# Optimization experiments

Measured on AMD Instinct MI355X. Metric: run time of the kernel, lower is better.

## Reference

```python
import jax, jax.numpy as jnp
import numpy as np

L, N, E, H = 2048, 4, 1024, 8


def setup_inputs() -> dict:
    key = jax.random.key(0)
    ks = jax.random.split(key, 5)
    s = 0.02
    x = jax.random.normal(ks[0], (L, N, E), dtype=jnp.float32)
    Wqkv = jax.random.normal(ks[1], (H, 3 * E, E), dtype=jnp.float32) * s
    bqkv = jnp.zeros((H, 3 * E), dtype=jnp.float32)
    Wo = jax.random.normal(ks[2], (H, E, E), dtype=jnp.float32) * s
    bo = jnp.zeros((H, E), dtype=jnp.float32)
    return {"x": x, "Wqkv": Wqkv, "bqkv": bqkv, "Wo": Wo, "bo": bo}


def reference(x, Wqkv, bqkv, Wo, bo):
    # x: [L, N, E]; each of H independent single-head attentions over full E,
    # outputs summed across heads (as in the torch module).
    scale = 1.0 / jnp.sqrt(jnp.asarray(E, dtype=x.dtype))
    # joint QKV projection per head: [H, L, N, 3E]
    qkv = jnp.einsum("lne,hfe->hlnf", x, Wqkv) + bqkv[:, None, None, :]
    q, k, v = jnp.split(qkv, 3, axis=-1)  # each [H, L, N, E]
    # scores over sequence: [H, N, L, L]
    scores = jnp.einsum("hlne,hmne->hnlm", q * scale, k)
    attn = jax.nn.softmax(scores, axis=-1)
    ctx = jnp.einsum("hnlm,hmne->hlne", attn, v)  # [H, L, N, E]
    out = jnp.einsum("hlne,hfe->hlnf", ctx, Wo) + bo[:, None, None, :]
    return out.sum(axis=0)  # [L, N, E]
```

## Files before the change

kernel.cpp:

```cpp
#include <hip/hip_runtime.h>

typedef __bf16 bf16;
typedef __bf16 bf16x4 __attribute__((ext_vector_type(4)));
typedef __bf16 bf16x8 __attribute__((ext_vector_type(8)));
typedef float f32x4 __attribute__((ext_vector_type(4)));
typedef unsigned int u32;
typedef unsigned short u16;

#define CL 2048
#define CN 4
#define CE 1024
#define CH 8

__device__ __forceinline__ void gload16(const bf16* g, bf16x8* l) {
  __builtin_amdgcn_global_load_lds((const __attribute__((address_space(1))) void*)g,
                                   (__attribute__((address_space(3))) void*)l, 16, 0, 0);
}

__device__ __forceinline__ void gemm_mainloop(
    const bf16* __restrict__ Abase, const bf16* __restrict__ Bbase,
    int lda, int ldb, int nk, bf16x8* As, bf16x8* Bs, f32x4 (&acc)[4][4])
{
  const int t = threadIdx.x;
  const int lane = t & 63;
  const int wid = t >> 6;
  const int wr = wid >> 1, wc = wid & 1;
  const int ln15 = lane & 15, kg = lane >> 4;

  int idxA[4], idxB[4];
#pragma unroll
  for (int i = 0; i < 4; ++i) {
    int lrow = wr*64 + i*16 + ln15;
    idxA[i] = lrow*4 + (kg ^ ((lrow >> 1) & 3));
    int lcol = wc*64 + i*16 + ln15;
    idxB[i] = lcol*4 + (kg ^ ((lcol >> 1) & 3));
  }
  const int r0 = t >> 2;         const int s0 = (t & 3) ^ ((r0 >> 1) & 3);
  const int r1 = (t + 256) >> 2; const int s1 = ((t + 256) & 3) ^ ((r1 >> 1) & 3);
  const bf16* a0 = Abase + (size_t)r0 * lda + s0 * 8;
  const bf16* a1 = Abase + (size_t)r1 * lda + s1 * 8;
  const bf16* b0 = Bbase + (size_t)r0 * ldb + s0 * 8;
  const bf16* b1 = Bbase + (size_t)r1 * ldb + s1 * 8;

  for (int kt = 0; kt < nk; ++kt) {
    gload16(a0 + kt * 32, &As[t]);
    gload16(a1 + kt * 32, &As[t + 256]);
    gload16(b0 + kt * 32, &Bs[t]);
    gload16(b1 + kt * 32, &Bs[t + 256]);
    __syncthreads();
    bf16x8 av[4], bv[4];
#pragma unroll
    for (int i = 0; i < 4; ++i) { av[i] = As[idxA[i]]; bv[i] = Bs[idxB[i]]; }
#pragma unroll
    for (int i = 0; i < 4; ++i)
#pragma unroll
      for (int j = 0; j < 4; ++j)
        acc[i][j] = __builtin_amdgcn_mfma_f32_16x16x32_bf16(av[i], bv[j], acc[i][j], 0, 0, 0);
    __syncthreads();
  }
}

__global__ void k_cast(const float4* __restrict__ in, bf16x4* __restrict__ out, int n4) {
  int i = blockIdx.x * 256 + threadIdx.x;
  if (i < n4) {
    float4 v = in[i];
    bf16x4 o = {(bf16)v.x, (bf16)v.y, (bf16)v.z, (bf16)v.w};
    out[i] = o;
  }
}

__global__ __launch_bounds__(256, 2)
void k_qkv(const bf16* __restrict__ xb, const bf16* __restrict__ Whb,
           const float* __restrict__ bqkv3,
           bf16* __restrict__ qb, bf16* __restrict__ kb, bf16* __restrict__ vb)
{
  __shared__ bf16x8 As[512], Bs[512];
  const int bm = blockIdx.x, bn = blockIdx.y;
  f32x4 acc[4][4] = {};
  const bf16* Ab = xb + (size_t)bm * 128 * CE;
  const bf16* Bb = Whb + (size_t)bn * 128 * CE;
  gemm_mainloop(Ab, Bb, CE, CE, CE / 32, As, Bs, acc);

  const int lane = threadIdx.x & 63, wid = threadIdx.x >> 6;
  const int wr = wid >> 1, wc = wid & 1, ln15 = lane & 15, lg = lane >> 4;
  const int f0 = bn * 128;
  bf16* dst; int e0; float scale = 1.0f;
  if (f0 < CE)          { dst = qb; e0 = f0;          scale = 0.03125f; }
  else if (f0 < 2 * CE) { dst = kb; e0 = f0 - CE; }
  else                  { dst = vb; e0 = f0 - 2 * CE; }
#pragma unroll
  for (int i = 0; i < 4; ++i)
#pragma unroll
    for (int r = 0; r < 4; ++r) {
      int m = bm * 128 + wr * 64 + i * 16 + lg * 4 + r;
      int l = m >> 2, n = m & 3;
      size_t rowbase = ((size_t)n * CL + l) * CE;
#pragma unroll
      for (int j = 0; j < 4; ++j) {
        int fo = wc * 64 + j * 16 + ln15;
        float v = acc[i][j][r] + bqkv3[f0 + fo];
        dst[rowbase + e0 + fo] = (bf16)(v * scale);
      }
    }
}

__global__ void k_transpose(const bf16* __restrict__ v, bf16* __restrict__ vt)
{
  __shared__ u16 s[64][66];
  const bf16* src = v + (size_t)blockIdx.z * CL * CE;
  bf16* dst = vt + (size_t)blockIdx.z * CE * CL;
  const int l0 = blockIdx.x * 64, e0 = blockIdx.y * 64;
  const int t = threadIdx.x;
#pragma unroll
  for (int rr = 0; rr < 2; ++rr) {
    int c = t + rr * 256;
    int row = c >> 3, cb = (c & 7) * 8;
    uint4 d = *(const uint4*)(src + (size_t)(l0 + row) * CE + e0 + cb);
    u32* sp = (u32*)&s[row][cb];
    sp[0] = d.x; sp[1] = d.y; sp[2] = d.z; sp[3] = d.w;
  }
  __syncthreads();
  const int erow = t >> 2, lc = (t & 3) * 16;
  u32 w[8];
#pragma unroll
  for (int q = 0; q < 8; ++q) {
    u16 a = s[lc + 2 * q][erow];
    u16 b = s[lc + 2 * q + 1][erow];
    w[q] = (u32)a | ((u32)b << 16);
  }
  bf16* dp = dst + (size_t)(e0 + erow) * CL + l0 + lc;
  ((uint4*)dp)[0] = make_uint4(w[0], w[1], w[2], w[3]);
  ((uint4*)dp)[1] = make_uint4(w[4], w[5], w[6], w[7]);
}

__global__ __launch_bounds__(256, 2)
void k_scores(const bf16* __restrict__ qb, const bf16* __restrict__ kb,
              bf16* __restrict__ S)
{
  __shared__ bf16x8 As[512], Bs[512];
  const int bm = blockIdx.x, bn = blockIdx.y, p = blockIdx.z;
  f32x4 acc[4][4] = {};
  const bf16* Ab = qb + (size_t)p * CL * CE + (size_t)bm * 128 * CE;
  const bf16* Bb = kb + (size_t)p * CL * CE + (size_t)bn * 128 * CE;
  gemm_mainloop(Ab, Bb, CE, CE, CE / 32, As, Bs, acc);

  const int lane = threadIdx.x & 63, wid = threadIdx.x >> 6;
  const int wr = wid >> 1, wc = wid & 1, ln15 = lane & 15, lg = lane >> 4;
  bf16* Sp = S + (size_t)p * CL * CL;
#pragma unroll
  for (int i = 0; i < 4; ++i)
#pragma unroll
    for (int r = 0; r < 4; ++r) {
      int row = bm * 128 + wr * 64 + i * 16 + lg * 4 + r;
#pragma unroll
      for (int j = 0; j < 4; ++j) {
        int col = bn * 128 + wc * 64 + j * 16 + ln15;
        Sp[(size_t)row * CL + col] = (bf16)acc[i][j][r];
      }
    }
}

__global__ __launch_bounds__(256)
void k_softmax(bf16* __restrict__ S)
{
  const int wid = threadIdx.x >> 6, lane = threadIdx.x & 63;
  const size_t row = (size_t)blockIdx.x * 4 + wid;
  ushort4* pv = (ushort4*)(S + row * CL);
  ushort4 d[8];
  float v[32];
#pragma unroll
  for (int c = 0; c < 8; ++c) d[c] = pv[c * 64 + lane];
#pragma unroll
  for (int c = 0; c < 8; ++c) {
    v[c*4+0] = __builtin_bit_cast(float, (u32)d[c].x << 16);
    v[c*4+1] = __builtin_bit_cast(float, (u32)d[c].y << 16);
    v[c*4+2] = __builtin_bit_cast(float, (u32)d[c].z << 16);
    v[c*4+3] = __builtin_bit_cast(float, (u32)d[c].w << 16);
  }
  float m = -1e30f;
#pragma unroll
  for (int i = 0; i < 32; ++i) m = fmaxf(m, v[i]);
#pragma unroll
  for (int o = 32; o; o >>= 1) m = fmaxf(m, __shfl_xor(m, o));
  float ssum = 0.f;
#pragma unroll
  for (int i = 0; i < 32; ++i) { v[i] = __expf(v[i] - m); ssum += v[i]; }
#pragma unroll
  for (int o = 32; o; o >>= 1) ssum += __shfl_xor(ssum, o);
  const float inv = 1.0f / ssum;
#pragma unroll
  for (int c = 0; c < 8; ++c) {
    ushort4 o;
    o.x = __builtin_bit_cast(u16, (bf16)(v[c*4+0] * inv));
    o.y = __builtin_bit_cast(u16, (bf16)(v[c*4+1] * inv));
    o.z = __builtin_bit_cast(u16, (bf16)(v[c*4+2] * inv));
    o.w = __builtin_bit_cast(u16, (bf16)(v[c*4+3] * inv));
    pv[c * 64 + lane] = o;
  }
}

__global__ __launch_bounds__(256, 2)
void k_pv(const bf16* __restrict__ S, const bf16* __restrict__ vt,
          bf16* __restrict__ ctx)
{
  __shared__ bf16x8 As[512], Bs[512];
  const int bm = blockIdx.x, bn = blockIdx.y, p = blockIdx.z;
  f32x4 acc[4][4] = {};
  const bf16* Ab = S + (size_t)p * CL * CL + (size_t)bm * 128 * CL;
  const bf16* Bb = vt + (size_t)p * CE * CL + (size_t)bn * 128 * CL;
  gemm_mainloop(Ab, Bb, CL, CL, CL / 32, As, Bs, acc);

  const int lane = threadIdx.x & 63, wid = threadIdx.x >> 6;
  const int wr = wid >> 1, wc = wid & 1, ln15 = lane & 15, lg = lane >> 4;
#pragma unroll
  for (int i = 0; i < 4; ++i)
#pragma unroll
    for (int r = 0; r < 4; ++r) {
      int l = bm * 128 + wr * 64 + i * 16 + lg * 4 + r;
      int m = l * 4 + p;
#pragma unroll
      for (int j = 0; j < 4; ++j) {
        int e = bn * 128 + wc * 64 + j * 16 + ln15;
        ctx[(size_t)m * CE + e] = (bf16)acc[i][j][r];
      }
    }
}

__global__ __launch_bounds__(256, 2)
void k_outproj(const bf16* __restrict__ ctx, const bf16* __restrict__ Wohb,
               const float* __restrict__ boh, float* __restrict__ out, int init)
{
  __shared__ bf16x8 As[512], Bs[512];
  const int bm = blockIdx.x, bn = blockIdx.y;
  f32x4 acc[4][4] = {};
  const bf16* Ab = ctx + (size_t)bm * 128 * CE;
  const bf16* Bb = Wohb + (size_t)bn * 128 * CE;
  gemm_mainloop(Ab, Bb, CE, CE, CE / 32, As, Bs, acc);

  const int lane = threadIdx.x & 63, wid = threadIdx.x >> 6;
  const int wr = wid >> 1, wc = wid & 1, ln15 = lane & 15, lg = lane >> 4;
#pragma unroll
  for (int i = 0; i < 4; ++i)
#pragma unroll
    for (int r = 0; r < 4; ++r) {
      int m = bm * 128 + wr * 64 + i * 16 + lg * 4 + r;
#pragma unroll
      for (int j = 0; j < 4; ++j) {
        int f = bn * 128 + wc * 64 + j * 16 + ln15;
        size_t idx = (size_t)m * CE + f;
        float prev = init ? 0.0f : out[idx];
        out[idx] = prev + acc[i][j][r] + boh[f];
      }
    }
}

extern "C" void kernel_launch(void* const* d_in, const int* in_sizes, int n_in,
                              void* d_out, int out_size, void* d_ws, size_t ws_size,
                              hipStream_t stream) {
  const float* x    = (const float*)d_in[0];
  const float* Wqkv = (const float*)d_in[1];
  const float* bqkv = (const float*)d_in[2];
  const float* Wo   = (const float*)d_in[3];
  const float* bo   = (const float*)d_in[4];
  float* out = (float*)d_out;

  bf16* xb   = (bf16*)d_ws;
  bf16* Whb  = xb   + (size_t)8192 * 1024;
  bf16* Wohb = Whb  + (size_t)3072 * 1024;
  bf16* qb   = Wohb + (size_t)1024 * 1024;
  bf16* kb   = qb   + (size_t)4 * 2048 * 1024;
  bf16* Sb   = kb   + (size_t)4 * 2048 * 1024;
  bf16* vtb  = Sb   + (size_t)4 * 2048 * 2048;
  bf16* vb   = Sb;
  bf16* ctx  = qb;

  const size_t needed = ((size_t)(8 + 3 + 1 + 8 + 8 + 16 + 8) * 1024 * 1024) * sizeof(bf16);
  if (ws_size < needed) return;

  k_cast<<<dim3(8192), 256, 0, stream>>>((const float4*)x, (bf16x4*)xb, 8192 * 1024 / 4);

  for (int h = 0; h < CH; ++h) {
    k_cast<<<dim3(3072), 256, 0, stream>>>((const float4*)(Wqkv + (size_t)h * 3072 * 1024),
                                           (bf16x4*)Whb, 3072 * 1024 / 4);
    k_cast<<<dim3(1024), 256, 0, stream>>>((const float4*)(Wo + (size_t)h * 1024 * 1024),
                                           (bf16x4*)Wohb, 1024 * 1024 / 4);
    k_qkv<<<dim3(64, 24), 256, 0, stream>>>(xb, Whb, bqkv + (size_t)h * 3 * CE, qb, kb, vb);
    k_transpose<<<dim3(32, 16, 4), 256, 0, stream>>>(vb, vtb);
    k_scores<<<dim3(16, 16, 4), 256, 0, stream>>>(qb, kb, Sb);
    k_softmax<<<dim3(2048), 256, 0, stream>>>(Sb);
    k_pv<<<dim3(16, 8, 4), 256, 0, stream>>>(Sb, vtb, ctx);
    k_outproj<<<dim3(64, 8), 256, 0, stream>>>(ctx, Wohb, bo + (size_t)h * CE, out, h == 0);
  }
}
```

Baseline: 1.917 ms.

## Use 256-row GEMM tiles with 4-stage async LDS prefetch pipeline

Replaces the shared single-buffered 128x128 GEMM mainloop with a templated 256xBN tile run by 512 threads (8 waves), with a 4-deep ring of LDS buffers filled by global_load_lds three k-steps ahead. Explicit vmcnt waits and a single barrier per k-step replace the two __syncthreads, and s_setprio raises priority around MFMA bursts. The aim is to hide global memory latency and raise data reuse per block. In exchange each block uses much more LDS and more accumulator registers, and the grids for the QKV, scores, PV and output-projection GEMMs become smaller, which can lower occupancy and leave fewer blocks to spread across CUs.

```diff
diff --git a/kernel.cpp b/kernel.cpp
--- a/kernel.cpp
+++ b/kernel.cpp
@@ -17,46 +17,97 @@
                                    (__attribute__((address_space(3))) void*)l, 16, 0, 0);
 }
 
-__device__ __forceinline__ void gemm_mainloop(
+template<int BN>
+__device__ __forceinline__ void gemm_mainloop256(
     const bf16* __restrict__ Abase, const bf16* __restrict__ Bbase,
-    int lda, int ldb, int nk, bf16x8* As, bf16x8* Bs, f32x4 (&acc)[4][4])
-{
+    int lda, int ldb, int nk, f32x4 (&acc)[8][BN / 64])
+{
+  constexpr int BJ = BN / 64;
+  constexpr int BCH = BN * 4;
+  __shared__ bf16x8 As[4][1024];
+  __shared__ bf16x8 Bs[4][BCH];
+
   const int t = threadIdx.x;
   const int lane = t & 63;
   const int wid = t >> 6;
-  const int wr = wid >> 1, wc = wid & 1;
+  const int wr = wid >> 2, wc = wid & 3;
   const int ln15 = lane & 15, kg = lane >> 4;
 
-  int idxA[4], idxB[4];
-#pragma unroll
-  for (int i = 0; i < 4; ++i) {
-    int lrow = wr*64 + i*16 + ln15;
-    idxA[i] = lrow*4 + (kg ^ ((lrow >> 1) & 3));
-    int lcol = wc*64 + i*16 + ln15;
-    idxB[i] = lcol*4 + (kg ^ ((lcol >> 1) & 3));
-  }
-  const int r0 = t >> 2;         const int s0 = (t & 3) ^ ((r0 >> 1) & 3);
-  const int r1 = (t + 256) >> 2; const int s1 = ((t + 256) & 3) ^ ((r1 >> 1) & 3);
-  const bf16* a0 = Abase + (size_t)r0 * lda + s0 * 8;
-  const bf16* a1 = Abase + (size_t)r1 * lda + s1 * 8;
-  const bf16* b0 = Bbase + (size_t)r0 * ldb + s0 * 8;
-  const bf16* b1 = Bbase + (size_t)r1 * ldb + s1 * 8;
+  int idxA[8], idxB[BJ];
+#pragma unroll
+  for (int i = 0; i < 8; ++i) {
+    int row = wr * 128 + i * 16 + ln15;
+    idxA[i] = row * 4 + (kg ^ ((row >> 1) & 3));
+  }
+#pragma unroll
+  for (int j = 0; j < BJ; ++j) {
+    int row = wc * (BN / 4) + j * 16 + ln15;
+    idxB[j] = row * 4 + (kg ^ ((row >> 1) & 3));
+  }
+
+  const int ra0 = t >> 2;          const int ca0 = (t & 3) ^ ((ra0 >> 1) & 3);
+  const int ra1 = (t + 512) >> 2;  const int ca1 = ((t + 512) & 3) ^ ((ra1 >> 1) & 3);
+  const bf16* aS0 = Abase + (size_t)ra0 * lda + ca0 * 8;
+  const bf16* aS1 = Abase + (size_t)ra1 * lda + ca1 * 8;
+  const bf16* bS0 = Bbase + (size_t)ra0 * ldb + ca0 * 8;
+  const bf16* bS1 = Bbase + (size_t)ra1 * ldb + ca1 * 8;
+
+#pragma unroll
+  for (int pt = 0; pt < 3; ++pt) {
+    gload16(aS0 + pt * 32, &As[pt][t]);
+    gload16(aS1 + pt * 32, &As[pt][t + 512]);
+    gload16(bS0 + pt * 32, &Bs[pt][t]);
+    if constexpr (BN == 256) gload16(bS1 + pt * 32, &Bs[pt][t + 512]);
+  }
 
   for (int kt = 0; kt < nk; ++kt) {
-    gload16(a0 + kt * 32, &As[t]);
-    gload16(a1 + kt * 32, &As[t + 256]);
-    gload16(b0 + kt * 32, &Bs[t]);
-    gload16(b1 + kt * 32, &Bs[t + 256]);
-    __syncthreads();
-    bf16x8 av[4], bv[4];
-#pragma unroll
-    for (int i = 0; i < 4; ++i) { av[i] = As[idxA[i]]; bv[i] = Bs[idxB[i]]; }
+    const int rem = nk - 1 - kt;
+    if constexpr (BN == 256) {
+      if (rem >= 2)      asm volatile("s_waitcnt vmcnt(8)" ::: "memory");
+      else if (rem == 1) asm volatile("s_waitcnt vmcnt(4)" ::: "memory");
+      else               asm volatile("s_waitcnt vmcnt(0)" ::: "memory");
+    } else {
+      if (rem >= 2)      asm volatile("s_waitcnt vmcnt(6)" ::: "memory");
+      else if (rem == 1) asm volatile("s_waitcnt vmcnt(3)" ::: "memory");
+      else               asm volatile("s_waitcnt vmcnt(0)" ::: "memory");
+    }
+    __builtin_amdgcn_s_barrier();
+
+    const int buf = kt & 3;
+    const int nbuf = (kt + 3) & 3;
+    const bool pf = (kt + 3) < nk;
+    const int ko = (kt + 3) * 32;
+
+    if (pf) {
+      gload16(aS0 + ko, &As[nbuf][t]);
+      gload16(aS1 + ko, &As[nbuf][t + 512]);
+    }
+    bf16x8 bv[BJ], av[4];
+#pragma unroll
+    for (int j = 0; j < BJ; ++j) bv[j] = Bs[buf][idxB[j]];
+#pragma unroll
+    for (int i = 0; i < 4; ++i) av[i] = As[buf][idxA[i]];
+    __builtin_amdgcn_s_setprio(1);
 #pragma unroll
     for (int i = 0; i < 4; ++i)
 #pragma unroll
-      for (int j = 0; j < 4; ++j)
+      for (int j = 0; j < BJ; ++j)
         acc[i][j] = __builtin_amdgcn_mfma_f32_16x16x32_bf16(av[i], bv[j], acc[i][j], 0, 0, 0);
-    __syncthreads();
+    __builtin_amdgcn_s_setprio(0);
+
+    if (pf) {
+      gload16(bS0 + ko, &Bs[nbuf][t]);
+      if constexpr (BN == 256) gload16(bS1 + ko, &Bs[nbuf][t + 512]);
+    }
+#pragma unroll
+    for (int i = 0; i < 4; ++i) av[i] = As[buf][idxA[i + 4]];
+    __builtin_amdgcn_s_setprio(1);
+#pragma unroll
+    for (int i = 0; i < 4; ++i)
+#pragma unroll
+      for (int j = 0; j < BJ; ++j)
+        acc[i + 4][j] = __builtin_amdgcn_mfma_f32_16x16x32_bf16(av[i], bv[j], acc[i + 4][j], 0, 0, 0);
+    __builtin_amdgcn_s_setprio(0);
   }
 }
 
@@ -69,35 +120,34 @@
   }
 }
 
-__global__ __launch_bounds__(256, 2)
+__global__ __launch_bounds__(512, 2)
 void k_qkv(const bf16* __restrict__ xb, const bf16* __restrict__ Whb,
            const float* __restrict__ bqkv3,
            bf16* __restrict__ qb, bf16* __restrict__ kb, bf16* __restrict__ vb)
 {
-  __shared__ bf16x8 As[512], Bs[512];
   const int bm = blockIdx.x, bn = blockIdx.y;
-  f32x4 acc[4][4] = {};
-  const bf16* Ab = xb + (size_t)bm * 128 * CE;
+  f32x4 acc[8][2] = {};
+  const bf16* Ab = xb + (size_t)bm * 256 * CE;
   const bf16* Bb = Whb + (size_t)bn * 128 * CE;
-  gemm_mainloop(Ab, Bb, CE, CE, CE / 32, As, Bs, acc);
+  gemm_mainloop256<128>(Ab, Bb, CE, CE, CE / 32, acc);
 
   const int lane = threadIdx.x & 63, wid = threadIdx.x >> 6;
-  const int wr = wid >> 1, wc = wid & 1, ln15 = lane & 15, lg = lane >> 4;
+  const int wr = wid >> 2, wc = wid & 3, ln15 = lane & 15, kg = lane >> 4;
   const int f0 = bn * 128;
   bf16* dst; int e0; float scale = 1.0f;
   if (f0 < CE)          { dst = qb; e0 = f0;          scale = 0.03125f; }
   else if (f0 < 2 * CE) { dst = kb; e0 = f0 - CE; }
   else                  { dst = vb; e0 = f0 - 2 * CE; }
 #pragma unroll
-  for (int i = 0; i < 4; ++i)
+  for (int i = 0; i < 8; ++i)
 #pragma unroll
     for (int r = 0; r < 4; ++r) {
-      int m = bm * 128 + wr * 64 + i * 16 + lg * 4 + r;
+      int m = bm * 256 + wr * 128 + i * 16 + kg * 4 + r;
       int l = m >> 2, n = m & 3;
       size_t rowbase = ((size_t)n * CL + l) * CE;
 #pragma unroll
-      for (int j = 0; j < 4; ++j) {
-        int fo = wc * 64 + j * 16 + ln15;
+      for (int j = 0; j < 2; ++j) {
+        int fo = wc * 32 + j * 16 + ln15;
         float v = acc[i][j][r] + bqkv3[f0 + fo];
         dst[rowbase + e0 + fo] = (bf16)(v * scale);
       }
@@ -133,28 +183,27 @@
   ((uint4*)dp)[1] = make_uint4(w[4], w[5], w[6], w[7]);
 }
 
-__global__ __launch_bounds__(256, 2)
+__global__ __launch_bounds__(512, 2)
 void k_scores(const bf16* __restrict__ qb, const bf16* __restrict__ kb,
               bf16* __restrict__ S)
 {
-  __shared__ bf16x8 As[512], Bs[512];
   const int bm = blockIdx.x, bn = blockIdx.y, p = blockIdx.z;
-  f32x4 acc[4][4] = {};
-  const bf16* Ab = qb + (size_t)p * CL * CE + (size_t)bm * 128 * CE;
-  const bf16* Bb = kb + (size_t)p * CL * CE + (size_t)bn * 128 * CE;
-  gemm_mainloop(Ab, Bb, CE, CE, CE / 32, As, Bs, acc);
+  f32x4 acc[8][4] = {};
+  const bf16* Ab = qb + (size_t)p * CL * CE + (size_t)bm * 256 * CE;
+  const bf16* Bb = kb + (size_t)p * CL * CE + (size_t)bn * 256 * CE;
+  gemm_mainloop256<256>(Ab, Bb, CE, CE, CE / 32, acc);
 
   const int lane = threadIdx.x & 63, wid = threadIdx.x >> 6;
-  const int wr = wid >> 1, wc = wid & 1, ln15 = lane & 15, lg = lane >> 4;
+  const int wr = wid >> 2, wc = wid & 3, ln15 = lane & 15, kg = lane >> 4;
   bf16* Sp = S + (size_t)p * CL * CL;
 #pragma unroll
-  for (int i = 0; i < 4; ++i)
+  for (int i = 0; i < 8; ++i)
 #pragma unroll
     for (int r = 0; r < 4; ++r) {
-      int row = bm * 128 + wr * 64 + i * 16 + lg * 4 + r;
+      int row = bm * 256 + wr * 128 + i * 16 + kg * 4 + r;
 #pragma unroll
       for (int j = 0; j < 4; ++j) {
-        int col = bn * 128 + wc * 64 + j * 16 + ln15;
+        int col = bn * 256 + wc * 64 + j * 16 + ln15;
         Sp[(size_t)row * CL + col] = (bf16)acc[i][j][r];
       }
     }
@@ -199,54 +248,52 @@
   }
 }
 
-__global__ __launch_bounds__(256, 2)
+__global__ __launch_bounds__(512, 2)
 void k_pv(const bf16* __restrict__ S, const bf16* __restrict__ vt,
           bf16* __restrict__ ctx)
 {
-  __shared__ bf16x8 As[512], Bs[512];
   const int bm = blockIdx.x, bn = blockIdx.y, p = blockIdx.z;
-  f32x4 acc[4][4] = {};
-  const bf16* Ab = S + (size_t)p * CL * CL + (size_t)bm * 128 * CL;
+  f32x4 acc[8][2] = {};
+  const bf16* Ab = S + (size_t)p * CL * CL + (size_t)bm * 256 * CL;
   const bf16* Bb = vt + (size_t)p * CE * CL + (size_t)bn * 128 * CL;
-  gemm_mainloop(Ab, Bb, CL, CL, CL / 32, As, Bs, acc);
+  gemm_mainloop256<128>(Ab, Bb, CL, CL, CL / 32, acc);
 
   const int lane = threadIdx.x & 63, wid = threadIdx.x >> 6;
-  const int wr = wid >> 1, wc = wid & 1, ln15 = lane & 15, lg = lane >> 4;
-#pragma unroll
-  for (int i = 0; i < 4; ++i)
+  const int wr = wid >> 2, wc = wid & 3, ln15 = lane & 15, kg = lane >> 4;
+#pragma unroll
+  for (int i = 0; i < 8; ++i)
 #pragma unroll
     for (int r = 0; r < 4; ++r) {
-      int l = bm * 128 + wr * 64 + i * 16 + lg * 4 + r;
+      int l = bm * 256 + wr * 128 + i * 16 + kg * 4 + r;
       int m = l * 4 + p;
 #pragma unroll
-      for (int j = 0; j < 4; ++j) {
-        int e = bn * 128 + wc * 64 + j * 16 + ln15;
+      for (int j = 0; j < 2; ++j) {
+        int e = bn * 128 + wc * 32 + j * 16 + ln15;
         ctx[(size_t)m * CE + e] = (bf16)acc[i][j][r];
       }
     }
 }
 
-__global__ __launch_bounds__(256, 2)
+__global__ __launch_bounds__(512, 2)
 void k_outproj(const bf16* __restrict__ ctx, const bf16* __restrict__ Wohb,
                const float* __restrict__ boh, float* __restrict__ out, int init)
 {
-  __shared__ bf16x8 As[512], Bs[512];
   const int bm = blockIdx.x, bn = blockIdx.y;
-  f32x4 acc[4][4] = {};
-  const bf16* Ab = ctx + (size_t)bm * 128 * CE;
+  f32x4 acc[8][2] = {};
+  const bf16* Ab = ctx + (size_t)bm * 256 * CE;
   const bf16* Bb = Wohb + (size_t)bn * 128 * CE;
-  gemm_mainloop(Ab, Bb, CE, CE, CE / 32, As, Bs, acc);
+  gemm_mainloop256<128>(Ab, Bb, CE, CE, CE / 32, acc);
 
   const int lane = threadIdx.x & 63, wid = threadIdx.x >> 6;
-  const int wr = wid >> 1, wc = wid & 1, ln15 = lane & 15, lg = lane >> 4;
-#pragma unroll
-  for (int i = 0; i < 4; ++i)
+  const int wr = wid >> 2, wc = wid & 3, ln15 = lane & 15, kg = lane >> 4;
+#pragma unroll
+  for (int i = 0; i < 8; ++i)
 #pragma unroll
     for (int r = 0; r < 4; ++r) {
-      int m = bm * 128 + wr * 64 + i * 16 + lg * 4 + r;
-#pragma unroll
-      for (int j = 0; j < 4; ++j) {
-        int f = bn * 128 + wc * 64 + j * 16 + ln15;
+      int m = bm * 256 + wr * 128 + i * 16 + kg * 4 + r;
+#pragma unroll
+      for (int j = 0; j < 2; ++j) {
+        int f = bn * 128 + wc * 32 + j * 16 + ln15;
         size_t idx = (size_t)m * CE + f;
         float prev = init ? 0.0f : out[idx];
         out[idx] = prev + acc[i][j][r] + boh[f];
@@ -284,11 +331,11 @@
                                            (bf16x4*)Whb, 3072 * 1024 / 4);
     k_cast<<<dim3(1024), 256, 0, stream>>>((const float4*)(Wo + (size_t)h * 1024 * 1024),
                                            (bf16x4*)Wohb, 1024 * 1024 / 4);
-    k_qkv<<<dim3(64, 24), 256, 0, stream>>>(xb, Whb, bqkv + (size_t)h * 3 * CE, qb, kb, vb);
+    k_qkv<<<dim3(32, 24), 512, 0, stream>>>(xb, Whb, bqkv + (size_t)h * 3 * CE, qb, kb, vb);
     k_transpose<<<dim3(32, 16, 4), 256, 0, stream>>>(vb, vtb);
-    k_scores<<<dim3(16, 16, 4), 256, 0, stream>>>(qb, kb, Sb);
+    k_scores<<<dim3(8, 8, 4), 512, 0, stream>>>(qb, kb, Sb);
     k_softmax<<<dim3(2048), 256, 0, stream>>>(Sb);
-    k_pv<<<dim3(16, 8, 4), 256, 0, stream>>>(Sb, vtb, ctx);
-    k_outproj<<<dim3(64, 8), 256, 0, stream>>>(ctx, Wohb, bo + (size_t)h * CE, out, h == 0);
-  }
-}
+    k_pv<<<dim3(8, 8, 4), 512, 0, stream>>>(Sb, vtb, ctx);
+    k_outproj<<<dim3(32, 8), 512, 0, stream>>>(ctx, Wohb, bo + (size_t)h * CE, out, h == 0);
+  }
+}
```

Result: slower. 2.109 ms (+10.0%).
